# Optimization experiments

Measured on AMD Instinct MI355X. Metric: run time of the kernel, lower is better.

Reference implementation:

```python
import jax, jax.numpy as jnp
import numpy as np

SIZE = 128
WIN = SIZE // 4   # sliding-window size == region size (32)
HALF = WIN // 2   # 16


def _conv(x, w, pad, groups=1):
    return jax.lax.conv_general_dilated(x, w, (1, 1), [(pad, pad), (pad, pad)],
        dimension_numbers=('NCHW', 'OIHW', 'NCHW'), feature_group_count=groups)


def _resize(x, h, w):
    # F.interpolate(..., mode='bilinear', align_corners=False)
    return jax.image.resize(x, (x.shape[0], x.shape[1], h, w), 'bilinear', antialias=False)


def _gauss_kernels():
    ax = np.linspace(-2.0, 2.0, 5)
    xx, yy = np.meshgrid(ax, ax)
    g = np.exp(-(xx ** 2 + yy ** 2) / 2.0) / (2.0 * np.pi)  # sigma = 1
    gx = (-xx * g).astype(np.float32)
    gy = (-yy * g).astype(np.float32)
    return (jnp.asarray(np.tile(gx[None, None], (3, 3, 1, 1))),
            jnp.asarray(np.tile(gy[None, None], (3, 3, 1, 1))))


def _edge_extract(x):
    Gx, Gy = _gauss_kernels()
    h = _conv(x, Gx, 2)
    v = _conv(x, Gy, 2)
    return jnp.tanh(jnp.sqrt(h * h + v * v + 1e-8))


def _color_moments(x, win=5):
    # F.unfold-based local mean / unbiased var / skewness, via depthwise box sums
    C = x.shape[1]
    n = float(win * win)
    ones = jnp.ones((C, 1, win, win), x.dtype)
    box = lambda z: _conv(z, ones, win // 2, groups=C)
    s1 = box(x); s2 = box(x * x); s3 = box(x * x * x)
    mean = s1 / n
    var = (s2 - n * mean * mean) / (n - 1.0)               # unbiased, matches torch.var
    m3 = (s3 - 3.0 * mean * s2 + 2.0 * n * mean ** 3) / n  # E[(x-m)^3]
    skew = m3 / (jnp.sqrt(jnp.maximum(var, 0.0)) ** 3 + 1e-6)
    return jnp.concatenate([mean, var, skew], 1)


def _locate_region(c):
    # scipy: gradient magnitude < 0.2 -> 4-connected label at argmax -> bbox center
    H, W = c.shape
    flat = jnp.argmax(c)
    xm = (flat // W).astype(jnp.int32)
    ym = (flat % W).astype(jnp.int32)
    gm = jnp.hypot(jnp.gradient(c, axis=0), jnp.gradient(c, axis=1))
    mask = gm < 0.2
    seed = jnp.zeros((H, W), bool).at[xm, ym].set(True) & mask

    def dil(r):
        d = r
        d = d | jnp.pad(r[1:, :], ((0, 1), (0, 0)))
        d = d | jnp.pad(r[:-1, :], ((1, 0), (0, 0)))
        d = d | jnp.pad(r[:, 1:], ((0, 0), (0, 1)))
        d = d | jnp.pad(r[:, :-1], ((0, 0), (1, 0)))
        return d & mask

    def body(s):
        r, _ = s
        nr = dil(r)
        return (nr, jnp.any(nr != r))

    region, _ = jax.lax.while_loop(lambda s: s[1], body, (seed, jnp.any(seed)))
    rows = jnp.any(region, 1); cols = jnp.any(region, 0)
    rs = jnp.argmax(rows); re = H - jnp.argmax(rows[::-1])
    cs = jnp.argmax(cols); ce = W - jnp.argmax(cols[::-1])
    ok = mask[xm, ym]  # label_at_max != 0
    x1 = jnp.where(ok, ((rs + re) // 2).astype(jnp.int32), xm)
    y1 = jnp.where(ok, ((cs + ce) // 2).astype(jnp.int32), ym)
    return x1, y1


def _affine_grid(move, H, W):
    # theta = [[1,0,tx],[0,1,ty]] with (tx,ty)=move, align_corners=False
    bx = (2.0 * jnp.arange(W, dtype=jnp.float32) + 1.0) / W - 1.0
    by = (2.0 * jnp.arange(H, dtype=jnp.float32) + 1.0) / H - 1.0
    gx = bx[None, None, :] + move[:, 0, None, None]
    gy = by[None, :, None] + move[:, 1, None, None]
    return jnp.stack(jnp.broadcast_arrays(gx, gy), -1)  # [B,H,W,2]


def _grid_sample(x, grid):
    # bilinear, zeros padding, align_corners=False (torch defaults)
    B, C, H, W = x.shape
    ix = ((grid[..., 0] + 1.0) * W - 1.0) / 2.0
    iy = ((grid[..., 1] + 1.0) * H - 1.0) / 2.0
    ix0 = jnp.floor(ix).astype(jnp.int32)
    iy0 = jnp.floor(iy).astype(jnp.int32)
    wx1 = ix - ix0; wy1 = iy - iy0
    b = jnp.arange(B)[:, None, None]

    def g(yy, xx):
        valid = ((xx >= 0) & (xx < W) & (yy >= 0) & (yy < H)).astype(x.dtype)
        v = x[b, :, jnp.clip(yy, 0, H - 1), jnp.clip(xx, 0, W - 1)]  # [B,Hg,Wg,C]
        return v * valid[..., None]

    out = (g(iy0, ix0) * ((1 - wy1) * (1 - wx1))[..., None]
         + g(iy0, ix0 + 1) * ((1 - wy1) * wx1)[..., None]
         + g(iy0 + 1, ix0) * (wy1 * (1 - wx1))[..., None]
         + g(iy0 + 1, ix0 + 1) * (wy1 * wx1)[..., None])
    return jnp.transpose(out, (0, 3, 1, 2))


def _bn_relu6(x, w, b):
    # BatchNorm2d in training mode (batch stats, biased var, eps=1e-5) + ReLU6
    m = x.mean((0, 2, 3), keepdims=True)
    v = ((x - m) ** 2).mean((0, 2, 3), keepdims=True)
    y = (x - m) / jnp.sqrt(v + 1e-5) * w[None, :, None, None] + b[None, :, None, None]
    return jnp.clip(y, 0.0, 6.0)


def setup_inputs():
    key = jax.random.key(0)
    ks = jax.random.split(key, 8)
    B, C = 8, 64
    return dict(
        warm_flag=1,
        feat1=jax.random.normal(ks[0], (B, C, SIZE, SIZE), jnp.float32),
        feat2=jax.random.normal(ks[1], (B, C, SIZE, SIZE), jnp.float32),
        cam1=jax.random.uniform(ks[2], (B, 64, 64), jnp.float32),
        cam2=jax.random.uniform(ks[3], (B, 64, 64), jnp.float32),
        f_g=jax.random.uniform(ks[4], (B, 3, 512, 512), jnp.float32),
        f_e=jax.random.uniform(ks[5], (B, 3, 512, 512), jnp.float32),
        conv1_w=jax.random.normal(ks[6], (C, 3, 3, 3), jnp.float32) * 0.1,
        conv1_b=jnp.zeros((C,), jnp.float32),
        conv2_w=jax.random.normal(ks[7], (C, 9, 3, 3), jnp.float32) * 0.1,
        conv2_b=jnp.zeros((C,), jnp.float32),
        bn_w=jnp.ones((C,), jnp.float32),
        bn_b=jnp.zeros((C,), jnp.float32),
    )


def reference(warm_flag, feat1, feat2, cam1, cam2, f_g, f_e,
              conv1_w, conv1_b, conv2_w, conv2_b, bn_w, bn_b):
    B = cam1.shape[0]
    c1 = _resize(cam1[:, None], SIZE, SIZE)
    c2 = _resize(cam2[:, None], SIZE, SIZE)

    if warm_flag == 1:
        # numpy/scipy path in torch is detached from autograd
        c1s = jax.lax.stop_gradient(c1)
        c2s = jax.lax.stop_gradient(c2)
        x1, y1 = jax.vmap(_locate_region)(c1s[:, 0])
        # valid-mode box convolution of cam2 with ones((H//4, W//4)), argmax
        box = jax.lax.conv_general_dilated(c2s, jnp.ones((1, 1, WIN, WIN), c2.dtype), (1, 1),
            'VALID', dimension_numbers=('NCHW', 'OIHW', 'NCHW'))[:, 0]
        Wv = box.shape[-1]
        flat = jnp.argmax(box.reshape(B, -1), -1)
        x2 = (flat // Wv + HALF).astype(jnp.int32)
        y2 = (flat % Wv + HALF).astype(jnp.int32)

        idx = jnp.arange(SIZE)
        def rect(xc, yc):
            r = (idx[None, :] >= jnp.maximum(xc - HALF, 0)[:, None]) & \
                (idx[None, :] < jnp.minimum(xc + HALF, SIZE)[:, None])
            cc = (idx[None, :] >= jnp.maximum(yc - HALF, 0)[:, None]) & \
                 (idx[None, :] < jnp.minimum(yc + HALF, SIZE)[:, None])
            return r[:, None, :, None] & cc[:, None, None, :]
        mask1 = rect(x1, y1).astype(feat1.dtype)
        mask2 = rect(x2, y2).astype(feat2.dtype)
        mi1 = jnp.stack([x1, y1], -1).astype(jnp.float32)
        mi2 = jnp.stack([x2, y2], -1).astype(jnp.float32)
    else:
        mask1 = jnp.zeros_like(feat1)
        mask2 = jnp.zeros_like(feat2)
        mi1 = jnp.zeros((B, 2), jnp.float32)
        mi2 = jnp.zeros((B, 2), jnp.float32)

    cam2_move = (mi2 - mi1) / (SIZE // 2)
    cam1_move = (mi1 - mi2) / (SIZE // 2)
    grid1 = _affine_grid(cam1_move, SIZE, SIZE)
    grid2 = _affine_grid(cam2_move, SIZE, SIZE)

    moments = _resize(_color_moments(f_e), SIZE, SIZE)   # [B,9,128,128]
    edge = _resize(_edge_extract(f_g), SIZE, SIZE)       # [B,3,128,128]
    feat1_edge = jnp.clip(_conv(edge, conv1_w, 1) + conv1_b[None, :, None, None], 0.0, 6.0)
    feat2_color = _conv(moments, conv2_w, 1) + conv2_b[None, :, None, None]

    feat2_move = _grid_sample(feat2_color * mask2, grid2)
    feat1_edge_move = _grid_sample(feat1_edge * mask1, grid1)

    Bc, C, H, W = feat1.shape
    f1 = feat1.reshape(Bc, C, -1)
    f2 = feat2.reshape(Bc, C, -1)
    f2m = feat2_move.reshape(Bc, C, -1)
    f1m = feat1_edge_move.reshape(Bc, C, -1)

    f2_attn = jax.nn.softmax(jnp.einsum('bcn,bdn->bcd', f2m, f1), -1)  # [B,C,C]
    feat1_apply = jnp.einsum('bcd,bdn->bcn', f2_attn, f1).reshape(Bc, C, H, W)
    f1_attn = jax.nn.softmax(jnp.einsum('bcn,bdn->bcd', f1m, f2), -1)
    feat2_apply = jnp.einsum('bcd,bdn->bcn', f1_attn, f2).reshape(Bc, C, H, W)

    feat1_apply = _bn_relu6(feat1_apply, bn_w, bn_b)
    feat2_apply = _bn_relu6(feat2_apply, bn_w, bn_b)

    if warm_flag == 0:
        return (feat1, feat2, grid1, grid2, feat1_edge, feat2_color, f1_attn, f2_attn, feat1, feat2)
    return (feat1_apply, feat2_apply, grid1, grid2, feat1_edge, feat2_color, f1_attn, f2_attn, feat1, feat2)
```

## Files before the change

### kernel.cpp

```cpp
#include <hip/hip_runtime.h>
#include <math.h>

#define SIZE 128
#define WIN 32
#define HALF 16
#define B 8
#define C 64
#define N (SIZE*SIZE)
#define BCN 8388608
#define BV 97

#define O_APPLY1   0
#define O_APPLY2   8388608
#define O_GRID1    16777216
#define O_GRID2    17039360
#define O_EDGEF    17301504
#define O_COLORF   25690112
#define O_ATTN1    34078720
#define O_ATTN2    34111488
#define O_FEAT1    34144256
#define O_FEAT2    42532864

#define WS_C1      0
#define WS_C2      131072
#define WS_COLSUM  262144
#define WS_XY      361472
#define WS_MOM     361600
#define WS_EDGE    1541248
#define WS_LOG1    1672320
#define WS_LOG2    1705088
#define WS_BN      1737856

#define NEGINF (-3.402823466e+38f)

typedef unsigned __int128 u128;

__global__ void k_init(float* __restrict__ p, int n) {
  int i = blockIdx.x * 256 + threadIdx.x;
  if (i < n) p[i] = 0.f;
}

__global__ __launch_bounds__(256) void k_resize_cam(
    const float* __restrict__ cam1, const float* __restrict__ cam2,
    float* __restrict__ c1, float* __restrict__ c2) {
  int idx = blockIdx.x * 256 + threadIdx.x;
  int which = idx >> 17;
  int rem = idx & 131071;
  int b = rem >> 14, i = (rem >> 7) & 127, j = rem & 127;
  const float* s = (which ? cam2 : cam1) + b * 4096;
  float fy = fminf(fmaxf(0.5f * (float)i - 0.25f, 0.f), 63.f);
  float fx = fminf(fmaxf(0.5f * (float)j - 0.25f, 0.f), 63.f);
  int y0 = (int)fy; float ty = fy - (float)y0; int y1i = min(y0 + 1, 63);
  int x0 = (int)fx; float tx = fx - (float)x0; int x1i = min(x0 + 1, 63);
  float v00 = s[y0 * 64 + x0],  v01 = s[y0 * 64 + x1i];
  float v10 = s[y1i * 64 + x0], v11 = s[y1i * 64 + x1i];
  float v = (1.f - ty) * ((1.f - tx) * v00 + tx * v01)
          + ty * ((1.f - tx) * v10 + tx * v11);
  (which ? c2 : c1)[rem] = v;
}

__device__ __forceinline__ u128 hfill(u128 g, u128 m) {
  u128 p = m;
  g |= p & (g << 1);  p &= p << 1;
  g |= p & (g << 2);  p &= p << 2;
  g |= p & (g << 4);  p &= p << 4;
  g |= p & (g << 8);  p &= p << 8;
  g |= p & (g << 16); p &= p << 16;
  g |= p & (g << 32); p &= p << 32;
  g |= p & (g << 64);
  p = m;
  g |= p & (g >> 1);  p &= p >> 1;
  g |= p & (g >> 2);  p &= p >> 2;
  g |= p & (g >> 4);  p &= p >> 4;
  g |= p & (g >> 8);  p &= p >> 8;
  g |= p & (g >> 16); p &= p >> 16;
  g |= p & (g >> 32); p &= p >> 32;
  g |= p & (g >> 64);
  return g;
}

__global__ __launch_bounds__(256) void k_locate(const float* __restrict__ c1,
                                                int* __restrict__ xy) {
  int b = blockIdx.x;
  const float* c = c1 + b * N;
  int tid = threadIdx.x;
  __shared__ float sc[N];
  __shared__ float sv[256]; __shared__ int si[256];
  __shared__ unsigned int maskw[512];
  __shared__ unsigned long long glo[128], ghi[128];
  __shared__ unsigned long long rowany[2];
  __shared__ int s_changed, s_xm, s_ym, s_ok;

  float bv = NEGINF; int bi = 0;
  const float4* c4 = (const float4*)c;
  float4* sc4 = (float4*)sc;
  #pragma unroll
  for (int k = 0; k < 16; ++k) {
    int i4 = k * 256 + tid;
    float4 v = c4[i4];
    sc4[i4] = v;
    int base = i4 * 4;
    if (v.x > bv) { bv = v.x; bi = base; }
    if (v.y > bv) { bv = v.y; bi = base + 1; }
    if (v.z > bv) { bv = v.z; bi = base + 2; }
    if (v.w > bv) { bv = v.w; bi = base + 3; }
  }
  sv[tid] = bv; si[tid] = bi;
  __syncthreads();
  for (int s = 128; s; s >>= 1) {
    if (tid < s) {
      float ov = sv[tid + s]; int oi = si[tid + s];
      if (ov > sv[tid] || (ov == sv[tid] && oi < si[tid])) { sv[tid] = ov; si[tid] = oi; }
    }
    __syncthreads();
  }
  if (tid == 0) { s_xm = si[0] >> 7; s_ym = si[0] & 127; }

  #pragma unroll
  for (int q = 0; q < 2; ++q) {
    int w = tid + q * 256;
    int row = w >> 2, cb = (w & 3) * 32;
    unsigned int m = 0;
    for (int bit = 0; bit < 32; ++bit) {
      int i = row, j = cb + bit;
      float gx_, gy_;
      if (i == 0)        gx_ = sc[128 + j] - sc[j];
      else if (i == 127) gx_ = sc[127 * 128 + j] - sc[126 * 128 + j];
      else               gx_ = 0.5f * (sc[(i + 1) * 128 + j] - sc[(i - 1) * 128 + j]);
      if (j == 0)        gy_ = sc[i * 128 + 1] - sc[i * 128];
      else if (j == 127) gy_ = sc[i * 128 + 127] - sc[i * 128 + 126];
      else               gy_ = 0.5f * (sc[i * 128 + j + 1] - sc[i * 128 + j - 1]);
      if (hypotf(gx_, gy_) < 0.2f) m |= (1u << bit);
    }
    maskw[w] = m;
  }
  __syncthreads();
  if (tid == 0) {
    int w = (s_xm << 2) + (s_ym >> 5), bit = s_ym & 31;
    s_ok = (maskw[w] >> bit) & 1;
  }
  __syncthreads();

  int r = tid;
  u128 m = 0, g = 0;
  if (tid < 128) {
    m = ((u128)maskw[r * 4])
      | ((u128)maskw[r * 4 + 1] << 32)
      | ((u128)maskw[r * 4 + 2] << 64)
      | ((u128)maskw[r * 4 + 3] << 96);
    if (s_ok && r == s_xm) g = ((u128)1) << s_ym;
    g = hfill(g, m);
  }
  for (;;) {
    if (tid == 0) s_changed = 0;
    if (tid < 128) { glo[r] = (unsigned long long)g; ghi[r] = (unsigned long long)(g >> 64); }
    __syncthreads();
    if (tid < 128) {
      u128 gn = g;
      if (r > 0)   gn |= ((u128)glo[r - 1]) | ((u128)ghi[r - 1] << 64);
      if (r < 127) gn |= ((u128)glo[r + 1]) | ((u128)ghi[r + 1] << 64);
      gn &= m;
      gn = hfill(gn, m);
      if (gn != g) { g = gn; s_changed = 1; }
    }
    __syncthreads();
    if (!s_changed) break;
  }

  if (tid < 128) {
    unsigned long long ba = __ballot(g != 0);
    if ((tid & 63) == 0) rowany[tid >> 6] = ba;
    glo[r] = (unsigned long long)g; ghi[r] = (unsigned long long)(g >> 64);
  }
  __syncthreads();
  if (tid == 0) {
    unsigned long long r0 = rowany[0], r1 = rowany[1];
    unsigned long long cl = 0, ch = 0;
    for (int i = 0; i < 128; ++i) { cl |= glo[i]; ch |= ghi[i]; }
    int rs = 0, re = 0, cs = 0, ce = 0;
    if (r0 | r1) {
      rs = r0 ? (__ffsll(r0) - 1) : 64 + (__ffsll(r1) - 1);
      re = r1 ? 128 - __clzll(r1) : 64 - __clzll(r0);
      cs = cl ? (__ffsll(cl) - 1) : 64 + (__ffsll(ch) - 1);
      ce = ch ? 128 - __clzll(ch) : 64 - __clzll(cl);
    }
    int x1, y1;
    if (s_ok) { x1 = (rs + re) >> 1; y1 = (cs + ce) >> 1; }
    else      { x1 = s_xm;           y1 = s_ym; }
    xy[b] = x1; xy[8 + b] = y1;
  }
}

__global__ __launch_bounds__(256) void k_colsum(const float* __restrict__ c2,
                                                float* __restrict__ cs) {
  int idx = blockIdx.x * 256 + threadIdx.x;
  if (idx >= B * BV * 128) return;
  int cc = idx & 127, r = (idx >> 7) % BV, b = idx / (BV * 128);
  const float* s = c2 + b * N + cc;
  float acc = 0.f;
  #pragma unroll
  for (int dy = 0; dy < WIN; ++dy) acc += s[(r + dy) * 128];
  cs[idx] = acc;
}

__global__ __launch_bounds__(256) void k_boxargmax(const float* __restrict__ colsum,
                                                   int* __restrict__ xy) {
  int b = blockIdx.x, tid = threadIdx.x;
  const float* cs = colsum + b * BV * 128;
  float bv = NEGINF; int bi = 0;
  for (int p = tid; p < BV * BV; p += 256) {
    int r = p / BV, cc = p % BV;
    const float* row = cs + r * 128 + cc;
    float s = 0.f;
    #pragma unroll
    for (int dx = 0; dx < WIN; ++dx) s += row[dx];
    if (s > bv) { bv = s; bi = p; }
  }
  __shared__ float sv[256]; __shared__ int si[256];
  sv[tid] = bv; si[tid] = bi;
  __syncthreads();
  for (int s = 128; s; s >>= 1) {
    if (tid < s) {
      float ov = sv[tid + s]; int oi = si[tid + s];
      if (ov > sv[tid] || (ov == sv[tid] && oi < si[tid])) { sv[tid] = ov; si[tid] = oi; }
    }
    __syncthreads();
  }
  if (tid == 0) { xy[16 + b] = si[0] / BV + HALF; xy[24 + b] = si[0] % BV + HALF; }
}

__global__ __launch_bounds__(256) void k_grids(const int* __restrict__ xy,
                                               float* __restrict__ g1, float* __restrict__ g2) {
  int idx = blockIdx.x * 256 + threadIdx.x;
  int b = idx >> 14, h = (idx >> 7) & 127, w = idx & 127;
  float x1 = (float)xy[b], y1 = (float)xy[8 + b];
  float x2 = (float)xy[16 + b], y2 = (float)xy[24 + b];
  float bx = (2.f * (float)w + 1.f) / 128.f - 1.f;
  float by = (2.f * (float)h + 1.f) / 128.f - 1.f;
  float m1x = (x1 - x2) / 64.f, m1y = (y1 - y2) / 64.f;
  g1[idx * 2]     = bx + m1x; g1[idx * 2 + 1] = by + m1y;
  g2[idx * 2]     = bx - m1x; g2[idx * 2 + 1] = by - m1y;
}

__global__ __launch_bounds__(256) void k_moments(const float* __restrict__ fe,
                                                 float* __restrict__ mom) {
  int blk = blockIdx.x;
  int tile = blk & 63, ch = (blk >> 6) % 3, b = blk / 192;
  int ti0 = (tile >> 3) * 16, tj0 = (tile & 7) * 16;
  const float* src = fe + (size_t)(b * 3 + ch) * 262144;
  __shared__ float sx[66 * 66];
  int oy0 = 4 * ti0 - 1, ox0 = 4 * tj0 - 1;
  int tid = threadIdx.x;
  for (int l = tid; l < 66 * 66; l += 256) {
    int r = l / 66, cc = l % 66;
    int gy = oy0 + r, gx = ox0 + cc;
    sx[l] = (gy >= 0 && gy < 512 && gx >= 0 && gx < 512) ? src[gy * 512 + gx] : 0.f;
  }
  __syncthreads();
  int ii = tid >> 4, jj = tid & 15;
  int i = ti0 + ii, j = tj0 + jj;
  float s1a[6], s2a[6], s3a[6], s1b[6], s2b[6], s3b[6];
  #pragma unroll
  for (int t = 0; t < 6; ++t) {
    float a1 = 0, a2 = 0, a3 = 0, b1 = 0, b2 = 0, b3 = 0;
    int lx = 4 * jj + t;
    #pragma unroll
    for (int r = 0; r < 6; ++r) {
      float v = sx[(4 * ii + r) * 66 + lx];
      float v2 = v * v, v3 = v2 * v;
      if (r < 5) { a1 += v; a2 += v2; a3 += v3; }
      if (r > 0) { b1 += v; b2 += v2; b3 += v3; }
    }
    s1a[t] = a1; s2a[t] = a2; s3a[t] = a3;
    s1b[t] = b1; s2b[t] = b2; s3b[t] = b3;
  }
  float am = 0, av = 0, as = 0;
  #pragma unroll
  for (int py = 0; py < 2; ++py) {
    #pragma unroll
    for (int px = 0; px < 2; ++px) {
      float s1 = 0, s2 = 0, s3 = 0;
      #pragma unroll
      for (int t = 0; t < 5; ++t) {
        s1 += py ? s1b[px + t] : s1a[px + t];
        s2 += py ? s2b[px + t] : s2a[px + t];
        s3 += py ? s3b[px + t] : s3a[px + t];
      }
      float mean = s1 / 25.f;
      float var  = (s2 - 25.f * mean * mean) / 24.f;
      float m3   = (s3 - 3.f * mean * s2 + 50.f * mean * mean * mean) / 25.f;
      float sq   = sqrtf(fmaxf(var, 0.f));
      float skew = m3 / (sq * sq * sq + 1e-6f);
      am += mean; av += var; as += skew;
    }
  }
  int base = (b * 9 + ch) * N + i * 128 + j;
  mom[base]         = 0.25f * am;
  mom[base + 3 * N] = 0.25f * av;
  mom[base + 6 * N] = 0.25f * as;
}

__global__ __launch_bounds__(256) void k_edge(const float* __restrict__ fg,
                                              float* __restrict__ edge) {
  int blk = blockIdx.x;
  int tile = blk & 63, b = blk >> 6;
  int ti0 = (tile >> 3) * 16, tj0 = (tile & 7) * 16;
  const float* s0 = fg + (size_t)b * 3 * 262144;
  __shared__ float sx[66 * 66];
  int oy0 = 4 * ti0 - 1, ox0 = 4 * tj0 - 1;
  int tid = threadIdx.x;
  for (int l = tid; l < 66 * 66; l += 256) {
    int r = l / 66, cc = l % 66;
    int gy = oy0 + r, gx = ox0 + cc;
    float v = 0.f;
    if (gy >= 0 && gy < 512 && gx >= 0 && gx < 512) {
      int o = gy * 512 + gx;
      v = s0[o] + s0[262144 + o] + s0[524288 + o];
    }
    sx[l] = v;
  }
  __syncthreads();
  int ii = tid >> 4, jj = tid & 15;
  int i = ti0 + ii, j = tj0 + jj;
  const float INV2PI = 0.15915494309189535f;
  float wg[5], ug[5];
  #pragma unroll
  for (int t = 0; t < 5; ++t) {
    float a = (float)t - 2.f;
    float e = expf(-0.5f * a * a);
    wg[t] = e; ug[t] = -a * e;
  }
  float rAa[6], rAb[6], rBa[6], rBb[6];
  #pragma unroll
  for (int t = 0; t < 6; ++t) {
    float aa = 0, ab = 0, ba = 0, bb = 0;
    int lx = 4 * jj + t;
    #pragma unroll
    for (int r = 0; r < 6; ++r) {
      float v = sx[(4 * ii + r) * 66 + lx];
      if (r < 5) { aa += v * wg[r]; ba += v * ug[r]; }
      if (r > 0) { ab += v * wg[r - 1]; bb += v * ug[r - 1]; }
    }
    rAa[t] = aa; rAb[t] = ab; rBa[t] = ba; rBb[t] = bb;
  }
  float acc = 0.f;
  #pragma unroll
  for (int py = 0; py < 2; ++py) {
    #pragma unroll
    for (int px = 0; px < 2; ++px) {
      float h = 0, v = 0;
      #pragma unroll
      for (int t = 0; t < 5; ++t) {
        float A  = py ? rAb[px + t] : rAa[px + t];
        float Bw = py ? rBb[px + t] : rBa[px + t];
        h += A * ug[t];
        v += Bw * wg[t];
      }
      h *= INV2PI; v *= INV2PI;
      acc += tanhf(sqrtf(h * h + v * v + 1e-8f));
    }
  }
  edge[b * N + i * 128 + j] = 0.25f * acc;
}

__global__ __launch_bounds__(256) void k_conv1(const float* __restrict__ edge,
                                               const float* __restrict__ w,
                                               const float* __restrict__ bias,
                                               float* __restrict__ out) {
  int b = blockIdx.x >> 6, tile = blockIdx.x & 63;
  int ti0 = (tile >> 3) * 16, tj0 = (tile & 7) * 16;
  __shared__ float et[18 * 18];
  __shared__ float ws1[64 * 12];
  int tid = threadIdx.x;
  for (int l = tid; l < 324; l += 256) {
    int r = l / 18, cc = l % 18;
    int gi = ti0 + r - 1, gj = tj0 + cc - 1;
    et[l] = (gi >= 0 && gi < 128 && gj >= 0 && gj < 128) ? edge[b * N + gi * 128 + gj] : 0.f;
  }
  for (int l = tid; l < 64 * 12; l += 256) {
    int o = l / 12, t = l % 12;
    ws1[l] = (t < 9) ? (w[o * 27 + t] + w[o * 27 + 9 + t] + w[o * 27 + 18 + t]) : 0.f;
  }
  __syncthreads();
  int i = tid >> 4, j = tid & 15;
  float win[12];
  #pragma unroll
  for (int dy = 0; dy < 3; ++dy)
    #pragma unroll
    for (int dx = 0; dx < 3; ++dx)
      win[dy * 3 + dx] = et[(i + dy) * 18 + (j + dx)];
  win[9] = 0.f; win[10] = 0.f; win[11] = 0.f;
  float* o = out + (size_t)b * C * N + (ti0 + i) * 128 + tj0 + j;
  for (int oc = 0; oc < C; ++oc) {
    const float4* wr = (const float4*)(ws1 + oc * 12);
    float acc = bias[oc];
    #pragma unroll
    for (int q = 0; q < 3; ++q) {
      float4 w4 = wr[q];
      acc += w4.x * win[4 * q] + w4.y * win[4 * q + 1]
           + w4.z * win[4 * q + 2] + w4.w * win[4 * q + 3];
    }
    o[oc * N] = fminf(fmaxf(acc, 0.f), 6.f);
  }
}

__global__ __launch_bounds__(256) void k_conv2(const float* __restrict__ mom,
                                               const float* __restrict__ w,
                                               const float* __restrict__ bias,
                                               float* __restrict__ out) {
  int b = blockIdx.x >> 6, tile = blockIdx.x & 63;
  int ti0 = (tile >> 3) * 16, tj0 = (tile & 7) * 16;
  __shared__ float mt[9 * 324];
  __shared__ float w2s[64 * 84];
  int tid = threadIdx.x;
  for (int l = tid; l < 9 * 324; l += 256) {
    int ic = l / 324, rem = l % 324, r = rem / 18, cc = rem % 18;
    int gi = ti0 + r - 1, gj = tj0 + cc - 1;
    mt[l] = (gi >= 0 && gi < 128 && gj >= 0 && gj < 128) ? mom[(b * 9 + ic) * N + gi * 128 + gj] : 0.f;
  }
  for (int l = tid; l < 64 * 84; l += 256) {
    int o = l / 84, t = l % 84;
    w2s[l] = (t < 81) ? w[o * 81 + t] : 0.f;
  }
  __syncthreads();
  int i = tid >> 4, j = tid & 15;
  float win[84];
  #pragma unroll
  for (int ic = 0; ic < 9; ++ic)
    #pragma unroll
    for (int dy = 0; dy < 3; ++dy)
      #pragma unroll
      for (int dx = 0; dx < 3; ++dx)
        win[ic * 9 + dy * 3 + dx] = mt[ic * 324 + (i + dy) * 18 + (j + dx)];
  win[81] = 0.f; win[82] = 0.f; win[83] = 0.f;
  float* o = out + (size_t)b * C * N + (ti0 + i) * 128 + tj0 + j;
  for (int oc = 0; oc < C; ++oc) {
    const float4* wr = (const float4*)(w2s + oc * 84);
    float acc = bias[oc];
    #pragma unroll
    for (int q = 0; q < 21; ++q) {
      float4 w4 = wr[q];
      acc += w4.x * win[4 * q] + w4.y * win[4 * q + 1]
           + w4.z * win[4 * q + 2] + w4.w * win[4 * q + 3];
    }
    o[oc * N] = acc;
  }
}

__global__ __launch_bounds__(256) void k_logits(const float* __restrict__ aB1,
                                                const float* __restrict__ bB1,
                                                float* __restrict__ out1,
                                                const float* __restrict__ aB2,
                                                const float* __restrict__ bB2,
                                                float* __restrict__ out2,
                                                const int* __restrict__ xy) {
  int mode = blockIdx.y;
  const float* aBase = mode ? aB2 : aB1;
  const float* bBase = mode ? bB2 : bB1;
  float* out = mode ? out2 : out1;
  int b = blockIdx.x >> 4, sl = blockIdx.x & 15;
  int x1 = xy[b], y1 = xy[8 + b], x2 = xy[16 + b], y2 = xy[24 + b];
  int dyh, dxw, rlo, rhi, clo, chi;
  if (mode == 0) {
    dyh = y1 - y2; dxw = x1 - x2;
    rlo = max(x1 - HALF, 0); rhi = min(x1 + HALF, SIZE);
    clo = max(y1 - HALF, 0); chi = min(y1 + HALF, SIZE);
  } else {
    dyh = y2 - y1; dxw = x2 - x1;
    rlo = max(x2 - HALF, 0); rhi = min(x2 + HALF, SIZE);
    clo = max(y2 - HALF, 0); chi = min(y2 + HALF, SIZE);
  }
  int hlo = max(0, rlo - dyh), hhi = min(SIZE, rhi - dyh);
  int wlo = max(0, clo - dxw), whi = min(SIZE, chi - dxw);
  int wn = whi - wlo, hn = hhi - hlo;
  int npos = (wn > 0 && hn > 0) ? wn * hn : 0;
  if (sl * 64 >= npos) return;

  __shared__ float aS[64][65];
  __shared__ float bS[64][65];
  int tid = threadIdx.x;
  const float* aB = aBase + (size_t)b * C * N;
  const float* bB = bBase + (size_t)b * C * N;
  for (int l = tid; l < 4096; l += 256) {
    int ch = l >> 6, k = l & 63;
    int p = sl * 64 + k;
    float av = 0.f, bv = 0.f;
    if (p < npos) {
      int h = hlo + p / wn, w = wlo + p % wn;
      av = aB[ch * N + (h + dyh) * 128 + (w + dxw)];
      bv = bB[ch * N + h * 128 + w];
    }
    aS[ch][k] = av; bS[ch][k] = bv;
  }
  __syncthreads();
  int ci = (tid >> 4) << 2, di = (tid & 15) << 2;
  float acc[4][4] = {};
  #pragma unroll 4
  for (int k = 0; k < 64; ++k) {
    float a0 = aS[ci][k], a1 = aS[ci + 1][k], a2 = aS[ci + 2][k], a3 = aS[ci + 3][k];
    float b0 = bS[di][k], b1 = bS[di + 1][k], b2 = bS[di + 2][k], b3 = bS[di + 3][k];
    acc[0][0] += a0 * b0; acc[0][1] += a0 * b1; acc[0][2] += a0 * b2; acc[0][3] += a0 * b3;
    acc[1][0] += a1 * b0; acc[1][1] += a1 * b1; acc[1][2] += a1 * b2; acc[1][3] += a1 * b3;
    acc[2][0] += a2 * b0; acc[2][1] += a2 * b1; acc[2][2] += a2 * b2; acc[2][3] += a2 * b3;
    acc[3][0] += a3 * b0; acc[3][1] += a3 * b1; acc[3][2] += a3 * b2; acc[3][3] += a3 * b3;
  }
  float* o = out + b * 4096;
  #pragma unroll
  for (int u = 0; u < 4; ++u)
    #pragma unroll
    for (int v = 0; v < 4; ++v)
      atomicAdd(&o[(ci + u) * 64 + (di + v)], acc[u][v]);
}

__global__ void k_softmax(const float* __restrict__ l1, const float* __restrict__ l2,
                          float* __restrict__ o6, float* __restrict__ o7) {
  int row = blockIdx.x;
  const float* src = blockIdx.y ? l2 : l1;
  float* dst = blockIdx.y ? o7 : o6;
  int lane = threadIdx.x;
  float v = src[row * 64 + lane];
  float mx = v;
  for (int off = 32; off; off >>= 1) mx = fmaxf(mx, __shfl_xor(mx, off));
  float e = expf(v - mx);
  float s = e;
  for (int off = 32; off; off >>= 1) s += __shfl_xor(s, off);
  dst[row * 64 + lane] = e / s;
}

__global__ __launch_bounds__(256) void k_apply(const float* __restrict__ a1,
                                               const float* __restrict__ s1_,
                                               float* __restrict__ d1,
                                               const float* __restrict__ a2,
                                               const float* __restrict__ s2_,
                                               float* __restrict__ d2) {
  const float* attn; const float* src; float* dst;
  if (blockIdx.y == 0) { attn = a1; src = s1_; dst = d1; }
  else                 { attn = a2; src = s2_; dst = d2; }
  int b = blockIdx.x >> 6, chunk = blockIdx.x & 63;
  int n0 = chunk * 256 + threadIdx.x;
  const float* s = src + (size_t)b * C * N + n0;
  float v[64];
  #pragma unroll
  for (int d = 0; d < 64; ++d) v[d] = s[d * N];
  const float4* at4 = (const float4*)(attn + b * 4096);
  float* o = dst + (size_t)b * C * N + n0;
  for (int c = 0; c < 64; ++c) {
    float acc = 0.f;
    #pragma unroll
    for (int q = 0; q < 16; ++q) {
      float4 w4 = at4[c * 16 + q];
      acc += w4.x * v[4 * q] + w4.y * v[4 * q + 1] + w4.z * v[4 * q + 2] + w4.w * v[4 * q + 3];
    }
    o[c * N] = acc;
  }
}

__global__ __launch_bounds__(256) void k_bnstats1(const float* __restrict__ t0,
                                                  const float* __restrict__ t1,
                                                  float* __restrict__ part) {
  int c = blockIdx.x, b = blockIdx.y, t = blockIdx.z;
  const float* src = (t ? t1 : t0) + (size_t)(b * C + c) * N;
  const float4* s4 = (const float4*)src;
  float s = 0.f, ss = 0.f;
  #pragma unroll
  for (int k = 0; k < 16; ++k) {
    float4 v = s4[k * 256 + threadIdx.x];
    s  += v.x + v.y + v.z + v.w;
    ss += v.x * v.x + v.y * v.y + v.z * v.z + v.w * v.w;
  }
  for (int off = 32; off; off >>= 1) {
    s  += __shfl_xor(s, off);
    ss += __shfl_xor(ss, off);
  }
  __shared__ float as[4], ass[4];
  int wave = threadIdx.x >> 6;
  if ((threadIdx.x & 63) == 0) { as[wave] = s; ass[wave] = ss; }
  __syncthreads();
  if (threadIdx.x == 0) {
    int idx = (t * C + c) * B + b;
    part[idx]        = as[0] + as[1] + as[2] + as[3];
    part[1024 + idx] = ass[0] + ass[1] + ass[2] + ass[3];
  }
}

__global__ void k_bnstats2(const float* __restrict__ part, float* __restrict__ stats) {
  int i = threadIdx.x;
  int t = i >> 6, c = i & 63;
  float s = 0.f, ss = 0.f;
  #pragma unroll
  for (int b = 0; b < B; ++b) {
    int idx = (t * C + c) * B + b;
    s  += part[idx];
    ss += part[1024 + idx];
  }
  float mean = s / 131072.f;
  float var  = ss / 131072.f - mean * mean;
  stats[t * 128 + c]      = mean;
  stats[t * 128 + 64 + c] = 1.f / sqrtf(var + 1e-5f);
}

__global__ __launch_bounds__(256) void k_bnapply(float* __restrict__ t0, float* __restrict__ t1,
                                                 const float* __restrict__ stats,
                                                 const float* __restrict__ bw,
                                                 const float* __restrict__ bb) {
  int e = blockIdx.x * 256 + threadIdx.x;
  int t = blockIdx.y;
  float* p = t ? t1 : t0;
  int c = (e >> 14) & 63;
  float m = stats[t * 128 + c], r = stats[t * 128 + 64 + c];
  float y = (p[e] - m) * r * bw[c] + bb[c];
  p[e] = fminf(fmaxf(y, 0.f), 6.f);
}

__global__ __launch_bounds__(256) void k_copy2(const float4* __restrict__ s1, float4* __restrict__ d1,
                                               const float4* __restrict__ s2, float4* __restrict__ d2) {
  int i = blockIdx.x * 256 + threadIdx.x;
  d1[i] = s1[i];
  d2[i] = s2[i];
}

extern "C" void kernel_launch(void* const* d_in, const int* in_sizes, int n_in,
                              void* d_out, int out_size, void* d_ws, size_t ws_size,
                              hipStream_t stream) {
  const float* feat1   = (const float*)d_in[1];
  const float* feat2   = (const float*)d_in[2];
  const float* cam1    = (const float*)d_in[3];
  const float* cam2    = (const float*)d_in[4];
  const float* f_g     = (const float*)d_in[5];
  const float* f_e     = (const float*)d_in[6];
  const float* conv1_w = (const float*)d_in[7];
  const float* conv1_b = (const float*)d_in[8];
  const float* conv2_w = (const float*)d_in[9];
  const float* conv2_b = (const float*)d_in[10];
  const float* bn_w    = (const float*)d_in[11];
  const float* bn_b    = (const float*)d_in[12];

  float* out = (float*)d_out;
  float* w = (float*)d_ws;
  int* xy = (int*)(w + WS_XY);

  float* o0 = out + O_APPLY1;
  float* o1 = out + O_APPLY2;
  float* o2 = out + O_GRID1;
  float* o3 = out + O_GRID2;
  float* o4 = out + O_EDGEF;
  float* o5 = out + O_COLORF;
  float* o6 = out + O_ATTN1;
  float* o7 = out + O_ATTN2;
  float* o8 = out + O_FEAT1;
  float* o9 = out + O_FEAT2;

  k_init<<<(65536 + 255) / 256, 256, 0, stream>>>(w + WS_LOG1, 65536);

  k_resize_cam<<<1024, 256, 0, stream>>>(cam1, cam2, w + WS_C1, w + WS_C2);
  k_locate<<<B, 256, 0, stream>>>(w + WS_C1, xy);
  k_colsum<<<(B * BV * 128 + 255) / 256, 256, 0, stream>>>(w + WS_C2, w + WS_COLSUM);
  k_boxargmax<<<B, 256, 0, stream>>>(w + WS_COLSUM, xy);
  k_grids<<<B * N / 256, 256, 0, stream>>>(xy, o2, o3);

  k_moments<<<B * 3 * 64, 256, 0, stream>>>(f_e, w + WS_MOM);
  k_edge<<<B * 64, 256, 0, stream>>>(f_g, w + WS_EDGE);
  k_conv1<<<B * 64, 256, 0, stream>>>(w + WS_EDGE, conv1_w, conv1_b, o4);
  k_conv2<<<B * 64, 256, 0, stream>>>(w + WS_MOM, conv2_w, conv2_b, o5);

  k_copy2<<<BCN / 4 / 256, 256, 0, stream>>>((const float4*)feat1, (float4*)o8,
                                             (const float4*)feat2, (float4*)o9);

  k_logits<<<dim3(B * 16, 2), 256, 0, stream>>>(o4, feat2, w + WS_LOG1,
                                                o5, feat1, w + WS_LOG2, xy);

  k_softmax<<<dim3(B * C, 2), 64, 0, stream>>>(w + WS_LOG1, w + WS_LOG2, o6, o7);

  k_apply<<<dim3(B * 64, 2), 256, 0, stream>>>(o7, feat1, o0, o6, feat2, o1);

  k_bnstats1<<<dim3(C, B, 2), 256, 0, stream>>>(o0, o1, w + WS_LOG1);
  k_bnstats2<<<1, 128, 0, stream>>>(w + WS_LOG1, w + WS_BN);

  k_bnapply<<<dim3(BCN / 256, 2), 256, 0, stream>>>(o0, o1, w + WS_BN, bn_w, bn_b);
}
```

Measured before the change: 640.6 us.

## Fuse front-end, prep, conv, BN-stats and copy kernels into fewer launches

Merges the camera resize, region locate, box-sum argmax and grid generation into one per-batch kernel that keeps everything in shared memory. It also combines the moments and edge kernels, and the two convs, into single launches. BN statistics are now accumulated inside the attention-apply kernel, which removes a full read pass over both outputs. The feature copy is folded into a vectorised BN apply. The front-end now runs on only 8 blocks with large shared memory, which may serialise work that was previously spread across the GPU.

```diff
diff --git a/kernel.cpp b/kernel.cpp
--- a/kernel.cpp
+++ b/kernel.cpp
@@ -21,43 +21,15 @@
 #define O_FEAT1    34144256
 #define O_FEAT2    42532864
 
-#define WS_C1      0
-#define WS_C2      131072
-#define WS_COLSUM  262144
+#define WS_BNP     0
 #define WS_XY      361472
 #define WS_MOM     361600
 #define WS_EDGE    1541248
-#define WS_LOG1    1672320
-#define WS_LOG2    1705088
 #define WS_BN      1737856
 
 #define NEGINF (-3.402823466e+38f)
 
 typedef unsigned __int128 u128;
-
-__global__ void k_init(float* __restrict__ p, int n) {
-  int i = blockIdx.x * 256 + threadIdx.x;
-  if (i < n) p[i] = 0.f;
-}
-
-__global__ __launch_bounds__(256) void k_resize_cam(
-    const float* __restrict__ cam1, const float* __restrict__ cam2,
-    float* __restrict__ c1, float* __restrict__ c2) {
-  int idx = blockIdx.x * 256 + threadIdx.x;
-  int which = idx >> 17;
-  int rem = idx & 131071;
-  int b = rem >> 14, i = (rem >> 7) & 127, j = rem & 127;
-  const float* s = (which ? cam2 : cam1) + b * 4096;
-  float fy = fminf(fmaxf(0.5f * (float)i - 0.25f, 0.f), 63.f);
-  float fx = fminf(fmaxf(0.5f * (float)j - 0.25f, 0.f), 63.f);
-  int y0 = (int)fy; float ty = fy - (float)y0; int y1i = min(y0 + 1, 63);
-  int x0 = (int)fx; float tx = fx - (float)x0; int x1i = min(x0 + 1, 63);
-  float v00 = s[y0 * 64 + x0],  v01 = s[y0 * 64 + x1i];
-  float v10 = s[y1i * 64 + x0], v11 = s[y1i * 64 + x1i];
-  float v = (1.f - ty) * ((1.f - tx) * v00 + tx * v01)
-          + ty * ((1.f - tx) * v10 + tx * v11);
-  (which ? c2 : c1)[rem] = v;
-}
 
 __device__ __forceinline__ u128 hfill(u128 g, u128 m) {
   u128 p = m;
@@ -79,31 +51,40 @@
   return g;
 }
 
-__global__ __launch_bounds__(256) void k_locate(const float* __restrict__ c1,
-                                                int* __restrict__ xy) {
-  int b = blockIdx.x;
-  const float* c = c1 + b * N;
-  int tid = threadIdx.x;
+__global__ __launch_bounds__(256) void k_front(
+    const float* __restrict__ cam1, const float* __restrict__ cam2,
+    int* __restrict__ xy, float* __restrict__ g1, float* __restrict__ g2) {
+  int b = blockIdx.x, tid = threadIdx.x;
   __shared__ float sc[N];
+  __shared__ float sc2[N];
   __shared__ float sv[256]; __shared__ int si[256];
   __shared__ unsigned int maskw[512];
   __shared__ unsigned long long glo[128], ghi[128];
   __shared__ unsigned long long rowany[2];
   __shared__ int s_changed, s_xm, s_ym, s_ok;
+  __shared__ int s_x1, s_y1, s_x2, s_y2;
+
+  const float* src1 = cam1 + b * 4096;
+  const float* src2 = cam2 + b * 4096;
 
   float bv = NEGINF; int bi = 0;
-  const float4* c4 = (const float4*)c;
-  float4* sc4 = (float4*)sc;
-  #pragma unroll
-  for (int k = 0; k < 16; ++k) {
-    int i4 = k * 256 + tid;
-    float4 v = c4[i4];
-    sc4[i4] = v;
-    int base = i4 * 4;
-    if (v.x > bv) { bv = v.x; bi = base; }
-    if (v.y > bv) { bv = v.y; bi = base + 1; }
-    if (v.z > bv) { bv = v.z; bi = base + 2; }
-    if (v.w > bv) { bv = v.w; bi = base + 3; }
+  for (int k = 0; k < 64; ++k) {
+    int pix = k * 256 + tid;
+    int i = pix >> 7, j = pix & 127;
+    float fy = fminf(fmaxf(0.5f * (float)i - 0.25f, 0.f), 63.f);
+    float fx = fminf(fmaxf(0.5f * (float)j - 0.25f, 0.f), 63.f);
+    int y0 = (int)fy; float ty = fy - (float)y0; int y1i = min(y0 + 1, 63);
+    int x0 = (int)fx; float tx = fx - (float)x0; int x1i = min(x0 + 1, 63);
+    float a00 = src1[y0 * 64 + x0],  a01 = src1[y0 * 64 + x1i];
+    float a10 = src1[y1i * 64 + x0], a11 = src1[y1i * 64 + x1i];
+    float v1 = (1.f - ty) * ((1.f - tx) * a00 + tx * a01)
+             + ty * ((1.f - tx) * a10 + tx * a11);
+    float c00 = src2[y0 * 64 + x0],  c01 = src2[y0 * 64 + x1i];
+    float c10 = src2[y1i * 64 + x0], c11 = src2[y1i * 64 + x1i];
+    float v2 = (1.f - ty) * ((1.f - tx) * c00 + tx * c01)
+             + ty * ((1.f - tx) * c10 + tx * c11);
+    sc[pix] = v1; sc2[pix] = v2;
+    if (v1 > bv) { bv = v1; bi = pix; }
   }
   sv[tid] = bv; si[tid] = bi;
   __syncthreads();
@@ -187,36 +168,27 @@
     int x1, y1;
     if (s_ok) { x1 = (rs + re) >> 1; y1 = (cs + ce) >> 1; }
     else      { x1 = s_xm;           y1 = s_ym; }
-    xy[b] = x1; xy[8 + b] = y1;
-  }
-}
-
-__global__ __launch_bounds__(256) void k_colsum(const float* __restrict__ c2,
-                                                float* __restrict__ cs) {
-  int idx = blockIdx.x * 256 + threadIdx.x;
-  if (idx >= B * BV * 128) return;
-  int cc = idx & 127, r = (idx >> 7) % BV, b = idx / (BV * 128);
-  const float* s = c2 + b * N + cc;
-  float acc = 0.f;
-  #pragma unroll
-  for (int dy = 0; dy < WIN; ++dy) acc += s[(r + dy) * 128];
-  cs[idx] = acc;
-}
-
-__global__ __launch_bounds__(256) void k_boxargmax(const float* __restrict__ colsum,
-                                                   int* __restrict__ xy) {
-  int b = blockIdx.x, tid = threadIdx.x;
-  const float* cs = colsum + b * BV * 128;
-  float bv = NEGINF; int bi = 0;
+    xy[b] = x1; xy[8 + b] = y1; s_x1 = x1; s_y1 = y1;
+  }
+  __syncthreads();
+
+  for (int idx = tid; idx < BV * 128; idx += 256) {
+    int rr = idx >> 7, cc = idx & 127;
+    float acc = 0.f;
+    #pragma unroll
+    for (int dy = 0; dy < WIN; ++dy) acc += sc2[(rr + dy) * 128 + cc];
+    sc[idx] = acc;
+  }
+  __syncthreads();
+
+  bv = NEGINF; bi = 0;
   for (int p = tid; p < BV * BV; p += 256) {
-    int r = p / BV, cc = p % BV;
-    const float* row = cs + r * 128 + cc;
+    int rr = p / BV, cc = p % BV;
     float s = 0.f;
     #pragma unroll
-    for (int dx = 0; dx < WIN; ++dx) s += row[dx];
+    for (int dx = 0; dx < WIN; ++dx) s += sc[rr * 128 + cc + dx];
     if (s > bv) { bv = s; bi = p; }
   }
-  __shared__ float sv[256]; __shared__ int si[256];
   sv[tid] = bv; si[tid] = bi;
   __syncthreads();
   for (int s = 128; s; s >>= 1) {
@@ -226,239 +198,237 @@
     }
     __syncthreads();
   }
-  if (tid == 0) { xy[16 + b] = si[0] / BV + HALF; xy[24 + b] = si[0] % BV + HALF; }
-}
-
-__global__ __launch_bounds__(256) void k_grids(const int* __restrict__ xy,
-                                               float* __restrict__ g1, float* __restrict__ g2) {
-  int idx = blockIdx.x * 256 + threadIdx.x;
-  int b = idx >> 14, h = (idx >> 7) & 127, w = idx & 127;
-  float x1 = (float)xy[b], y1 = (float)xy[8 + b];
-  float x2 = (float)xy[16 + b], y2 = (float)xy[24 + b];
-  float bx = (2.f * (float)w + 1.f) / 128.f - 1.f;
-  float by = (2.f * (float)h + 1.f) / 128.f - 1.f;
-  float m1x = (x1 - x2) / 64.f, m1y = (y1 - y2) / 64.f;
-  g1[idx * 2]     = bx + m1x; g1[idx * 2 + 1] = by + m1y;
-  g2[idx * 2]     = bx - m1x; g2[idx * 2 + 1] = by - m1y;
-}
-
-__global__ __launch_bounds__(256) void k_moments(const float* __restrict__ fe,
-                                                 float* __restrict__ mom) {
-  int blk = blockIdx.x;
-  int tile = blk & 63, ch = (blk >> 6) % 3, b = blk / 192;
-  int ti0 = (tile >> 3) * 16, tj0 = (tile & 7) * 16;
-  const float* src = fe + (size_t)(b * 3 + ch) * 262144;
+  if (tid == 0) {
+    int x2 = si[0] / BV + HALF, y2 = si[0] % BV + HALF;
+    xy[16 + b] = x2; xy[24 + b] = y2; s_x2 = x2; s_y2 = y2;
+  }
+  __syncthreads();
+
+  float x1f = (float)s_x1, y1f = (float)s_y1;
+  float x2f = (float)s_x2, y2f = (float)s_y2;
+  float m1x = (x1f - x2f) / 64.f, m1y = (y1f - y2f) / 64.f;
+  float* g1b = g1 + (size_t)b * N * 2;
+  float* g2b = g2 + (size_t)b * N * 2;
+  for (int k = 0; k < 64; ++k) {
+    int pix = k * 256 + tid;
+    int h = pix >> 7, w = pix & 127;
+    float bx = (2.f * (float)w + 1.f) / 128.f - 1.f;
+    float by = (2.f * (float)h + 1.f) / 128.f - 1.f;
+    g1b[pix * 2]     = bx + m1x; g1b[pix * 2 + 1] = by + m1y;
+    g2b[pix * 2]     = bx - m1x; g2b[pix * 2 + 1] = by - m1y;
+  }
+}
+
+__global__ __launch_bounds__(256) void k_prep(const float* __restrict__ fe,
+                                              const float* __restrict__ fg,
+                                              float* __restrict__ mom,
+                                              float* __restrict__ edge) {
   __shared__ float sx[66 * 66];
-  int oy0 = 4 * ti0 - 1, ox0 = 4 * tj0 - 1;
   int tid = threadIdx.x;
-  for (int l = tid; l < 66 * 66; l += 256) {
-    int r = l / 66, cc = l % 66;
-    int gy = oy0 + r, gx = ox0 + cc;
-    sx[l] = (gy >= 0 && gy < 512 && gx >= 0 && gx < 512) ? src[gy * 512 + gx] : 0.f;
-  }
-  __syncthreads();
-  int ii = tid >> 4, jj = tid & 15;
-  int i = ti0 + ii, j = tj0 + jj;
-  float s1a[6], s2a[6], s3a[6], s1b[6], s2b[6], s3b[6];
-  #pragma unroll
-  for (int t = 0; t < 6; ++t) {
-    float a1 = 0, a2 = 0, a3 = 0, b1 = 0, b2 = 0, b3 = 0;
-    int lx = 4 * jj + t;
-    #pragma unroll
-    for (int r = 0; r < 6; ++r) {
-      float v = sx[(4 * ii + r) * 66 + lx];
-      float v2 = v * v, v3 = v2 * v;
-      if (r < 5) { a1 += v; a2 += v2; a3 += v3; }
-      if (r > 0) { b1 += v; b2 += v2; b3 += v3; }
-    }
-    s1a[t] = a1; s2a[t] = a2; s3a[t] = a3;
-    s1b[t] = b1; s2b[t] = b2; s3b[t] = b3;
-  }
-  float am = 0, av = 0, as = 0;
-  #pragma unroll
-  for (int py = 0; py < 2; ++py) {
-    #pragma unroll
-    for (int px = 0; px < 2; ++px) {
-      float s1 = 0, s2 = 0, s3 = 0;
-      #pragma unroll
-      for (int t = 0; t < 5; ++t) {
-        s1 += py ? s1b[px + t] : s1a[px + t];
-        s2 += py ? s2b[px + t] : s2a[px + t];
-        s3 += py ? s3b[px + t] : s3a[px + t];
+  if (blockIdx.x < 1536) {
+    int blk = blockIdx.x;
+    int tile = blk & 63, ch = (blk >> 6) % 3, b = blk / 192;
+    int ti0 = (tile >> 3) * 16, tj0 = (tile & 7) * 16;
+    const float* src = fe + (size_t)(b * 3 + ch) * 262144;
+    int oy0 = 4 * ti0 - 1, ox0 = 4 * tj0 - 1;
+    for (int l = tid; l < 66 * 66; l += 256) {
+      int r = l / 66, cc = l % 66;
+      int gy = oy0 + r, gx = ox0 + cc;
+      sx[l] = (gy >= 0 && gy < 512 && gx >= 0 && gx < 512) ? src[gy * 512 + gx] : 0.f;
+    }
+    __syncthreads();
+    int ii = tid >> 4, jj = tid & 15;
+    int i = ti0 + ii, j = tj0 + jj;
+    float s1a[6], s2a[6], s3a[6], s1b[6], s2b[6], s3b[6];
+    #pragma unroll
+    for (int t = 0; t < 6; ++t) {
+      float a1 = 0, a2 = 0, a3 = 0, b1 = 0, b2 = 0, b3 = 0;
+      int lx = 4 * jj + t;
+      #pragma unroll
+      for (int r = 0; r < 6; ++r) {
+        float v = sx[(4 * ii + r) * 66 + lx];
+        float v2 = v * v, v3 = v2 * v;
+        if (r < 5) { a1 += v; a2 += v2; a3 += v3; }
+        if (r > 0) { b1 += v; b2 += v2; b3 += v3; }
       }
-      float mean = s1 / 25.f;
-      float var  = (s2 - 25.f * mean * mean) / 24.f;
-      float m3   = (s3 - 3.f * mean * s2 + 50.f * mean * mean * mean) / 25.f;
-      float sq   = sqrtf(fmaxf(var, 0.f));
-      float skew = m3 / (sq * sq * sq + 1e-6f);
-      am += mean; av += var; as += skew;
-    }
-  }
-  int base = (b * 9 + ch) * N + i * 128 + j;
-  mom[base]         = 0.25f * am;
-  mom[base + 3 * N] = 0.25f * av;
-  mom[base + 6 * N] = 0.25f * as;
-}
-
-__global__ __launch_bounds__(256) void k_edge(const float* __restrict__ fg,
-                                              float* __restrict__ edge) {
-  int blk = blockIdx.x;
-  int tile = blk & 63, b = blk >> 6;
-  int ti0 = (tile >> 3) * 16, tj0 = (tile & 7) * 16;
-  const float* s0 = fg + (size_t)b * 3 * 262144;
-  __shared__ float sx[66 * 66];
-  int oy0 = 4 * ti0 - 1, ox0 = 4 * tj0 - 1;
-  int tid = threadIdx.x;
-  for (int l = tid; l < 66 * 66; l += 256) {
-    int r = l / 66, cc = l % 66;
-    int gy = oy0 + r, gx = ox0 + cc;
-    float v = 0.f;
-    if (gy >= 0 && gy < 512 && gx >= 0 && gx < 512) {
-      int o = gy * 512 + gx;
-      v = s0[o] + s0[262144 + o] + s0[524288 + o];
-    }
-    sx[l] = v;
-  }
-  __syncthreads();
-  int ii = tid >> 4, jj = tid & 15;
-  int i = ti0 + ii, j = tj0 + jj;
-  const float INV2PI = 0.15915494309189535f;
-  float wg[5], ug[5];
-  #pragma unroll
-  for (int t = 0; t < 5; ++t) {
-    float a = (float)t - 2.f;
-    float e = expf(-0.5f * a * a);
-    wg[t] = e; ug[t] = -a * e;
-  }
-  float rAa[6], rAb[6], rBa[6], rBb[6];
-  #pragma unroll
-  for (int t = 0; t < 6; ++t) {
-    float aa = 0, ab = 0, ba = 0, bb = 0;
-    int lx = 4 * jj + t;
-    #pragma unroll
-    for (int r = 0; r < 6; ++r) {
-      float v = sx[(4 * ii + r) * 66 + lx];
-      if (r < 5) { aa += v * wg[r]; ba += v * ug[r]; }
-      if (r > 0) { ab += v * wg[r - 1]; bb += v * ug[r - 1]; }
-    }
-    rAa[t] = aa; rAb[t] = ab; rBa[t] = ba; rBb[t] = bb;
-  }
-  float acc = 0.f;
-  #pragma unroll
-  for (int py = 0; py < 2; ++py) {
-    #pragma unroll
-    for (int px = 0; px < 2; ++px) {
-      float h = 0, v = 0;
-      #pragma unroll
-      for (int t = 0; t < 5; ++t) {
-        float A  = py ? rAb[px + t] : rAa[px + t];
-        float Bw = py ? rBb[px + t] : rBa[px + t];
-        h += A * ug[t];
-        v += Bw * wg[t];
+      s1a[t] = a1; s2a[t] = a2; s3a[t] = a3;
+      s1b[t] = b1; s2b[t] = b2; s3b[t] = b3;
+    }
+    float am = 0, av = 0, as = 0;
+    #pragma unroll
+    for (int py = 0; py < 2; ++py) {
+      #pragma unroll
+      for (int px = 0; px < 2; ++px) {
+        float s1 = 0, s2 = 0, s3 = 0;
+        #pragma unroll
+        for (int t = 0; t < 5; ++t) {
+          s1 += py ? s1b[px + t] : s1a[px + t];
+          s2 += py ? s2b[px + t] : s2a[px + t];
+          s3 += py ? s3b[px + t] : s3a[px + t];
+        }
+        float mean = s1 / 25.f;
+        float var  = (s2 - 25.f * mean * mean) / 24.f;
+        float m3   = (s3 - 3.f * mean * s2 + 50.f * mean * mean * mean) / 25.f;
+        float sq   = sqrtf(fmaxf(var, 0.f));
+        float skew = m3 / (sq * sq * sq + 1e-6f);
+        am += mean; av += var; as += skew;
       }
-      h *= INV2PI; v *= INV2PI;
-      acc += tanhf(sqrtf(h * h + v * v + 1e-8f));
-    }
-  }
-  edge[b * N + i * 128 + j] = 0.25f * acc;
-}
-
-__global__ __launch_bounds__(256) void k_conv1(const float* __restrict__ edge,
-                                               const float* __restrict__ w,
-                                               const float* __restrict__ bias,
-                                               float* __restrict__ out) {
+    }
+    int base = (b * 9 + ch) * N + i * 128 + j;
+    mom[base]         = 0.25f * am;
+    mom[base + 3 * N] = 0.25f * av;
+    mom[base + 6 * N] = 0.25f * as;
+  } else {
+    int blk = blockIdx.x - 1536;
+    int tile = blk & 63, b = blk >> 6;
+    int ti0 = (tile >> 3) * 16, tj0 = (tile & 7) * 16;
+    const float* s0 = fg + (size_t)b * 3 * 262144;
+    int oy0 = 4 * ti0 - 1, ox0 = 4 * tj0 - 1;
+    for (int l = tid; l < 66 * 66; l += 256) {
+      int r = l / 66, cc = l % 66;
+      int gy = oy0 + r, gx = ox0 + cc;
+      float v = 0.f;
+      if (gy >= 0 && gy < 512 && gx >= 0 && gx < 512) {
+        int o = gy * 512 + gx;
+        v = s0[o] + s0[262144 + o] + s0[524288 + o];
+      }
+      sx[l] = v;
+    }
+    __syncthreads();
+    int ii = tid >> 4, jj = tid & 15;
+    int i = ti0 + ii, j = tj0 + jj;
+    const float INV2PI = 0.15915494309189535f;
+    float wg[5], ug[5];
+    #pragma unroll
+    for (int t = 0; t < 5; ++t) {
+      float a = (float)t - 2.f;
+      float e = expf(-0.5f * a * a);
+      wg[t] = e; ug[t] = -a * e;
+    }
+    float rAa[6], rAb[6], rBa[6], rBb[6];
+    #pragma unroll
+    for (int t = 0; t < 6; ++t) {
+      float aa = 0, ab = 0, ba = 0, bb = 0;
+      int lx = 4 * jj + t;
+      #pragma unroll
+      for (int r = 0; r < 6; ++r) {
+        float v = sx[(4 * ii + r) * 66 + lx];
+        if (r < 5) { aa += v * wg[r]; ba += v * ug[r]; }
+        if (r > 0) { ab += v * wg[r - 1]; bb += v * ug[r - 1]; }
+      }
+      rAa[t] = aa; rAb[t] = ab; rBa[t] = ba; rBb[t] = bb;
+    }
+    float acc = 0.f;
+    #pragma unroll
+    for (int py = 0; py < 2; ++py) {
+      #pragma unroll
+      for (int px = 0; px < 2; ++px) {
+        float h = 0, v = 0;
+        #pragma unroll
+        for (int t = 0; t < 5; ++t) {
+          float A  = py ? rAb[px + t] : rAa[px + t];
+          float Bw = py ? rBb[px + t] : rBa[px + t];
+          h += A * ug[t];
+          v += Bw * wg[t];
+        }
+        h *= INV2PI; v *= INV2PI;
+        acc += tanhf(sqrtf(h * h + v * v + 1e-8f));
+      }
+    }
+    edge[b * N + i * 128 + j] = 0.25f * acc;
+  }
+}
+
+__global__ __launch_bounds__(256) void k_conv12(
+    const float* __restrict__ edge, const float* __restrict__ w1,
+    const float* __restrict__ b1, float* __restrict__ o4,
+    const float* __restrict__ mom, const float* __restrict__ w2,
+    const float* __restrict__ b2, float* __restrict__ o5) {
+  __shared__ float tin[9 * 324];
+  __shared__ float wsm[64 * 84];
   int b = blockIdx.x >> 6, tile = blockIdx.x & 63;
   int ti0 = (tile >> 3) * 16, tj0 = (tile & 7) * 16;
-  __shared__ float et[18 * 18];
-  __shared__ float ws1[64 * 12];
   int tid = threadIdx.x;
-  for (int l = tid; l < 324; l += 256) {
-    int r = l / 18, cc = l % 18;
-    int gi = ti0 + r - 1, gj = tj0 + cc - 1;
-    et[l] = (gi >= 0 && gi < 128 && gj >= 0 && gj < 128) ? edge[b * N + gi * 128 + gj] : 0.f;
-  }
-  for (int l = tid; l < 64 * 12; l += 256) {
-    int o = l / 12, t = l % 12;
-    ws1[l] = (t < 9) ? (w[o * 27 + t] + w[o * 27 + 9 + t] + w[o * 27 + 18 + t]) : 0.f;
-  }
-  __syncthreads();
   int i = tid >> 4, j = tid & 15;
-  float win[12];
-  #pragma unroll
-  for (int dy = 0; dy < 3; ++dy)
-    #pragma unroll
-    for (int dx = 0; dx < 3; ++dx)
-      win[dy * 3 + dx] = et[(i + dy) * 18 + (j + dx)];
-  win[9] = 0.f; win[10] = 0.f; win[11] = 0.f;
-  float* o = out + (size_t)b * C * N + (ti0 + i) * 128 + tj0 + j;
-  for (int oc = 0; oc < C; ++oc) {
-    const float4* wr = (const float4*)(ws1 + oc * 12);
-    float acc = bias[oc];
-    #pragma unroll
-    for (int q = 0; q < 3; ++q) {
-      float4 w4 = wr[q];
-      acc += w4.x * win[4 * q] + w4.y * win[4 * q + 1]
-           + w4.z * win[4 * q + 2] + w4.w * win[4 * q + 3];
-    }
-    o[oc * N] = fminf(fmaxf(acc, 0.f), 6.f);
-  }
-}
-
-__global__ __launch_bounds__(256) void k_conv2(const float* __restrict__ mom,
-                                               const float* __restrict__ w,
-                                               const float* __restrict__ bias,
-                                               float* __restrict__ out) {
-  int b = blockIdx.x >> 6, tile = blockIdx.x & 63;
-  int ti0 = (tile >> 3) * 16, tj0 = (tile & 7) * 16;
-  __shared__ float mt[9 * 324];
-  __shared__ float w2s[64 * 84];
-  int tid = threadIdx.x;
-  for (int l = tid; l < 9 * 324; l += 256) {
-    int ic = l / 324, rem = l % 324, r = rem / 18, cc = rem % 18;
-    int gi = ti0 + r - 1, gj = tj0 + cc - 1;
-    mt[l] = (gi >= 0 && gi < 128 && gj >= 0 && gj < 128) ? mom[(b * 9 + ic) * N + gi * 128 + gj] : 0.f;
-  }
-  for (int l = tid; l < 64 * 84; l += 256) {
-    int o = l / 84, t = l % 84;
-    w2s[l] = (t < 81) ? w[o * 81 + t] : 0.f;
-  }
-  __syncthreads();
-  int i = tid >> 4, j = tid & 15;
-  float win[84];
-  #pragma unroll
-  for (int ic = 0; ic < 9; ++ic)
+  if (blockIdx.y == 0) {
+    for (int l = tid; l < 324; l += 256) {
+      int r = l / 18, cc = l % 18;
+      int gi = ti0 + r - 1, gj = tj0 + cc - 1;
+      tin[l] = (gi >= 0 && gi < 128 && gj >= 0 && gj < 128) ? edge[b * N + gi * 128 + gj] : 0.f;
+    }
+    for (int l = tid; l < 64 * 12; l += 256) {
+      int o = l / 12, t = l % 12;
+      wsm[l] = (t < 9) ? (w1[o * 27 + t] + w1[o * 27 + 9 + t] + w1[o * 27 + 18 + t]) : 0.f;
+    }
+    __syncthreads();
+    float win[12];
     #pragma unroll
     for (int dy = 0; dy < 3; ++dy)
       #pragma unroll
       for (int dx = 0; dx < 3; ++dx)
-        win[ic * 9 + dy * 3 + dx] = mt[ic * 324 + (i + dy) * 18 + (j + dx)];
-  win[81] = 0.f; win[82] = 0.f; win[83] = 0.f;
-  float* o = out + (size_t)b * C * N + (ti0 + i) * 128 + tj0 + j;
-  for (int oc = 0; oc < C; ++oc) {
-    const float4* wr = (const float4*)(w2s + oc * 84);
-    float acc = bias[oc];
-    #pragma unroll
-    for (int q = 0; q < 21; ++q) {
-      float4 w4 = wr[q];
-      acc += w4.x * win[4 * q] + w4.y * win[4 * q + 1]
-           + w4.z * win[4 * q + 2] + w4.w * win[4 * q + 3];
-    }
-    o[oc * N] = acc;
+        win[dy * 3 + dx] = tin[(i + dy) * 18 + (j + dx)];
+    win[9] = 0.f; win[10] = 0.f; win[11] = 0.f;
+    float* o = o4 + (size_t)b * C * N + (ti0 + i) * 128 + tj0 + j;
+    for (int oc = 0; oc < C; ++oc) {
+      const float4* wr = (const float4*)(wsm + oc * 12);
+      float acc = b1[oc];
+      #pragma unroll
+      for (int q = 0; q < 3; ++q) {
+        float4 w4 = wr[q];
+        acc += w4.x * win[4 * q] + w4.y * win[4 * q + 1]
+             + w4.z * win[4 * q + 2] + w4.w * win[4 * q + 3];
+      }
+      o[oc * N] = fminf(fmaxf(acc, 0.f), 6.f);
+    }
+  } else {
+    for (int l = tid; l < 9 * 324; l += 256) {
+      int ic = l / 324, rem = l % 324, r = rem / 18, cc = rem % 18;
+      int gi = ti0 + r - 1, gj = tj0 + cc - 1;
+      tin[l] = (gi >= 0 && gi < 128 && gj >= 0 && gj < 128) ? mom[(b * 9 + ic) * N + gi * 128 + gj] : 0.f;
+    }
+    for (int l = tid; l < 64 * 84; l += 256) {
+      int o = l / 84, t = l % 84;
+      wsm[l] = (t < 81) ? w2[o * 81 + t] : 0.f;
+    }
+    __syncthreads();
+    float win[84];
+    #pragma unroll
+    for (int ic = 0; ic < 9; ++ic)
+      #pragma unroll
+      for (int dy = 0; dy < 3; ++dy)
+        #pragma unroll
+        for (int dx = 0; dx < 3; ++dx)
+          win[ic * 9 + dy * 3 + dx] = tin[ic * 324 + (i + dy) * 18 + (j + dx)];
+    win[81] = 0.f; win[82] = 0.f; win[83] = 0.f;
+    float* o = o5 + (size_t)b * C * N + (ti0 + i) * 128 + tj0 + j;
+    for (int oc = 0; oc < C; ++oc) {
+      const float4* wr = (const float4*)(wsm + oc * 84);
+      float acc = b2[oc];
+      #pragma unroll
+      for (int q = 0; q < 21; ++q) {
+        float4 w4 = wr[q];
+        acc += w4.x * win[4 * q] + w4.y * win[4 * q + 1]
+             + w4.z * win[4 * q + 2] + w4.w * win[4 * q + 3];
+      }
+      o[oc * N] = acc;
+    }
   }
 }
 
 __global__ __launch_bounds__(256) void k_logits(const float* __restrict__ aB1,
                                                 const float* __restrict__ bB1,
-                                                float* __restrict__ out1,
                                                 const float* __restrict__ aB2,
                                                 const float* __restrict__ bB2,
-                                                float* __restrict__ out2,
+                                                float* __restrict__ lg,
                                                 const int* __restrict__ xy) {
   int mode = blockIdx.y;
   const float* aBase = mode ? aB2 : aB1;
   const float* bBase = mode ? bB2 : bB1;
-  float* out = mode ? out2 : out1;
   int b = blockIdx.x >> 4, sl = blockIdx.x & 15;
+  int tid = threadIdx.x;
+  int ci = (tid >> 4) << 2, di = (tid & 15) << 2;
+  float* o = lg + (size_t)(((mode * 8 + b) * 16 + sl)) * 4096;
+
   int x1 = xy[b], y1 = xy[8 + b], x2 = xy[16 + b], y2 = xy[24 + b];
   int dyh, dxw, rlo, rhi, clo, chi;
   if (mode == 0) {
@@ -474,11 +444,17 @@
   int wlo = max(0, clo - dxw), whi = min(SIZE, chi - dxw);
   int wn = whi - wlo, hn = hhi - hlo;
   int npos = (wn > 0 && hn > 0) ? wn * hn : 0;
-  if (sl * 64 >= npos) return;
+  if (sl * 64 >= npos) {
+    #pragma unroll
+    for (int u = 0; u < 4; ++u)
+      #pragma unroll
+      for (int v = 0; v < 4; ++v)
+        o[(ci + u) * 64 + (di + v)] = 0.f;
+    return;
+  }
 
   __shared__ float aS[64][65];
   __shared__ float bS[64][65];
-  int tid = threadIdx.x;
   const float* aB = aBase + (size_t)b * C * N;
   const float* bB = bBase + (size_t)b * C * N;
   for (int l = tid; l < 4096; l += 256) {
@@ -493,32 +469,34 @@
     aS[ch][k] = av; bS[ch][k] = bv;
   }
   __syncthreads();
-  int ci = (tid >> 4) << 2, di = (tid & 15) << 2;
   float acc[4][4] = {};
   #pragma unroll 4
   for (int k = 0; k < 64; ++k) {
     float a0 = aS[ci][k], a1 = aS[ci + 1][k], a2 = aS[ci + 2][k], a3 = aS[ci + 3][k];
-    float b0 = bS[di][k], b1 = bS[di + 1][k], b2 = bS[di + 2][k], b3 = bS[di + 3][k];
-    acc[0][0] += a0 * b0; acc[0][1] += a0 * b1; acc[0][2] += a0 * b2; acc[0][3] += a0 * b3;
-    acc[1][0] += a1 * b0; acc[1][1] += a1 * b1; acc[1][2] += a1 * b2; acc[1][3] += a1 * b3;
-    acc[2][0] += a2 * b0; acc[2][1] += a2 * b1; acc[2][2] += a2 * b2; acc[2][3] += a2 * b3;
-    acc[3][0] += a3 * b0; acc[3][1] += a3 * b1; acc[3][2] += a3 * b2; acc[3][3] += a3 * b3;
-  }
-  float* o = out + b * 4096;
+    float b0 = bS[di][k], b1v = bS[di + 1][k], b2v = bS[di + 2][k], b3 = bS[di + 3][k];
+    acc[0][0] += a0 * b0; acc[0][1] += a0 * b1v; acc[0][2] += a0 * b2v; acc[0][3] += a0 * b3;
+    acc[1][0] += a1 * b0; acc[1][1] += a1 * b1v; acc[1][2] += a1 * b2v; acc[1][3] += a1 * b3;
+    acc[2][0] += a2 * b0; acc[2][1] += a2 * b1v; acc[2][2] += a2 * b2v; acc[2][3] += a2 * b3;
+    acc[3][0] += a3 * b0; acc[3][1] += a3 * b1v; acc[3][2] += a3 * b2v; acc[3][3] += a3 * b3;
+  }
   #pragma unroll
   for (int u = 0; u < 4; ++u)
     #pragma unroll
     for (int v = 0; v < 4; ++v)
-      atomicAdd(&o[(ci + u) * 64 + (di + v)], acc[u][v]);
-}
-
-__global__ void k_softmax(const float* __restrict__ l1, const float* __restrict__ l2,
+      o[(ci + u) * 64 + (di + v)] = acc[u][v];
+}
+
+__global__ void k_softmax(const float* __restrict__ lg,
                           float* __restrict__ o6, float* __restrict__ o7) {
   int row = blockIdx.x;
-  const float* src = blockIdx.y ? l2 : l1;
-  float* dst = blockIdx.y ? o7 : o6;
+  int mode = blockIdx.y;
+  float* dst = mode ? o7 : o6;
+  int b = row >> 6, c = row & 63;
   int lane = threadIdx.x;
-  float v = src[row * 64 + lane];
+  const float* base = lg + (size_t)((mode * 8 + b) * 16) * 4096 + c * 64 + lane;
+  float v = 0.f;
+  #pragma unroll
+  for (int sl = 0; sl < 16; ++sl) v += base[sl * 4096];
   float mx = v;
   for (int off = 32; off; off >>= 1) mx = fmaxf(mx, __shfl_xor(mx, off));
   float e = expf(v - mx);
@@ -527,15 +505,17 @@
   dst[row * 64 + lane] = e / s;
 }
 
-__global__ __launch_bounds__(256) void k_apply(const float* __restrict__ a1,
-                                               const float* __restrict__ s1_,
-                                               float* __restrict__ d1,
-                                               const float* __restrict__ a2,
-                                               const float* __restrict__ s2_,
-                                               float* __restrict__ d2) {
+__global__ __launch_bounds__(256) void k_applyst(const float* __restrict__ a1,
+                                                 const float* __restrict__ s1_,
+                                                 float* __restrict__ d1,
+                                                 const float* __restrict__ a2,
+                                                 const float* __restrict__ s2_,
+                                                 float* __restrict__ d2,
+                                                 float* __restrict__ bnp) {
   const float* attn; const float* src; float* dst;
-  if (blockIdx.y == 0) { attn = a1; src = s1_; dst = d1; }
-  else                 { attn = a2; src = s2_; dst = d2; }
+  int t = blockIdx.y;
+  if (t == 0) { attn = a1; src = s1_; dst = d1; }
+  else        { attn = a2; src = s2_; dst = d2; }
   int b = blockIdx.x >> 6, chunk = blockIdx.x & 63;
   int n0 = chunk * 256 + threadIdx.x;
   const float* s = src + (size_t)b * C * N + n0;
@@ -544,6 +524,8 @@
   for (int d = 0; d < 64; ++d) v[d] = s[d * N];
   const float4* at4 = (const float4*)(attn + b * 4096);
   float* o = dst + (size_t)b * C * N + n0;
+  __shared__ float red[64][4], red2[64][4];
+  int lane = threadIdx.x & 63, wave = threadIdx.x >> 6;
   for (int c = 0; c < 64; ++c) {
     float acc = 0.f;
     #pragma unroll
@@ -552,71 +534,66 @@
       acc += w4.x * v[4 * q] + w4.y * v[4 * q + 1] + w4.z * v[4 * q + 2] + w4.w * v[4 * q + 3];
     }
     o[c * N] = acc;
-  }
-}
-
-__global__ __launch_bounds__(256) void k_bnstats1(const float* __restrict__ t0,
-                                                  const float* __restrict__ t1,
-                                                  float* __restrict__ part) {
-  int c = blockIdx.x, b = blockIdx.y, t = blockIdx.z;
-  const float* src = (t ? t1 : t0) + (size_t)(b * C + c) * N;
-  const float4* s4 = (const float4*)src;
+    float sr = acc, ssr = acc * acc;
+    for (int off = 32; off; off >>= 1) {
+      sr  += __shfl_xor(sr, off);
+      ssr += __shfl_xor(ssr, off);
+    }
+    if (lane == 0) { red[c][wave] = sr; red2[c][wave] = ssr; }
+  }
+  __syncthreads();
+  if (threadIdx.x < 64) {
+    int c = threadIdx.x;
+    float sr  = red[c][0] + red[c][1] + red[c][2] + red[c][3];
+    float ssr = red2[c][0] + red2[c][1] + red2[c][2] + red2[c][3];
+    int idx = (t * 64 + c) * 512 + blockIdx.x;
+    bnp[idx]         = sr;
+    bnp[65536 + idx] = ssr;
+  }
+}
+
+__global__ void k_bnstats2(const float* __restrict__ bnp, float* __restrict__ stats) {
+  __shared__ float sr[128][4], ssr[128][4];
+  int tid = threadIdx.x;
+  int combo = tid >> 2, q = tid & 3;
   float s = 0.f, ss = 0.f;
-  #pragma unroll
-  for (int k = 0; k < 16; ++k) {
-    float4 v = s4[k * 256 + threadIdx.x];
-    s  += v.x + v.y + v.z + v.w;
-    ss += v.x * v.x + v.y * v.y + v.z * v.z + v.w * v.w;
-  }
-  for (int off = 32; off; off >>= 1) {
-    s  += __shfl_xor(s, off);
-    ss += __shfl_xor(ss, off);
-  }
-  __shared__ float as[4], ass[4];
-  int wave = threadIdx.x >> 6;
-  if ((threadIdx.x & 63) == 0) { as[wave] = s; ass[wave] = ss; }
-  __syncthreads();
-  if (threadIdx.x == 0) {
-    int idx = (t * C + c) * B + b;
-    part[idx]        = as[0] + as[1] + as[2] + as[3];
-    part[1024 + idx] = ass[0] + ass[1] + ass[2] + ass[3];
-  }
-}
-
-__global__ void k_bnstats2(const float* __restrict__ part, float* __restrict__ stats) {
-  int i = threadIdx.x;
-  int t = i >> 6, c = i & 63;
-  float s = 0.f, ss = 0.f;
-  #pragma unroll
-  for (int b = 0; b < B; ++b) {
-    int idx = (t * C + c) * B + b;
-    s  += part[idx];
-    ss += part[1024 + idx];
-  }
-  float mean = s / 131072.f;
-  float var  = ss / 131072.f - mean * mean;
-  stats[t * 128 + c]      = mean;
-  stats[t * 128 + 64 + c] = 1.f / sqrtf(var + 1e-5f);
-}
-
-__global__ __launch_bounds__(256) void k_bnapply(float* __restrict__ t0, float* __restrict__ t1,
-                                                 const float* __restrict__ stats,
-                                                 const float* __restrict__ bw,
-                                                 const float* __restrict__ bb) {
-  int e = blockIdx.x * 256 + threadIdx.x;
+  for (int k = 0; k < 128; ++k) {
+    int idx = combo * 512 + q * 128 + k;
+    s  += bnp[idx];
+    ss += bnp[65536 + idx];
+  }
+  sr[combo][q] = s; ssr[combo][q] = ss;
+  __syncthreads();
+  if (q == 0) {
+    float S  = sr[combo][0] + sr[combo][1] + sr[combo][2] + sr[combo][3];
+    float SS = ssr[combo][0] + ssr[combo][1] + ssr[combo][2] + ssr[combo][3];
+    int t = combo >> 6, c = combo & 63;
+    float mean = S / 131072.f;
+    float var  = SS / 131072.f - mean * mean;
+    stats[t * 128 + c]      = mean;
+    stats[t * 128 + 64 + c] = 1.f / sqrtf(var + 1e-5f);
+  }
+}
+
+__global__ __launch_bounds__(256) void k_final(
+    const float4* __restrict__ f1, float4* __restrict__ o8,
+    const float4* __restrict__ f2, float4* __restrict__ o9,
+    float4* __restrict__ o0, float4* __restrict__ o1,
+    const float* __restrict__ stats,
+    const float* __restrict__ bw, const float* __restrict__ bb) {
+  int i = blockIdx.x * 256 + threadIdx.x;
   int t = blockIdx.y;
-  float* p = t ? t1 : t0;
-  int c = (e >> 14) & 63;
+  if (t == 0) o8[i] = f1[i]; else o9[i] = f2[i];
+  float4* p = t ? o1 : o0;
+  int c = (i >> 12) & 63;
   float m = stats[t * 128 + c], r = stats[t * 128 + 64 + c];
-  float y = (p[e] - m) * r * bw[c] + bb[c];
-  p[e] = fminf(fmaxf(y, 0.f), 6.f);
-}
-
-__global__ __launch_bounds__(256) void k_copy2(const float4* __restrict__ s1, float4* __restrict__ d1,
-                                               const float4* __restrict__ s2, float4* __restrict__ d2) {
-  int i = blockIdx.x * 256 + threadIdx.x;
-  d1[i] = s1[i];
-  d2[i] = s2[i];
+  float w_ = bw[c], b_ = bb[c];
+  float4 v = p[i];
+  v.x = fminf(fmaxf((v.x - m) * r * w_ + b_, 0.f), 6.f);
+  v.y = fminf(fmaxf((v.y - m) * r * w_ + b_, 0.f), 6.f);
+  v.z = fminf(fmaxf((v.z - m) * r * w_ + b_, 0.f), 6.f);
+  v.w = fminf(fmaxf((v.w - m) * r * w_ + b_, 0.f), 6.f);
+  p[i] = v;
 }
 
 extern "C" void kernel_launch(void* const* d_in, const int* in_sizes, int n_in,
@@ -650,31 +627,24 @@
   float* o8 = out + O_FEAT1;
   float* o9 = out + O_FEAT2;
 
-  k_init<<<(65536 + 255) / 256, 256, 0, stream>>>(w + WS_LOG1, 65536);
-
-  k_resize_cam<<<1024, 256, 0, stream>>>(cam1, cam2, w + WS_C1, w + WS_C2);
-  k_locate<<<B, 256, 0, stream>>>(w + WS_C1, xy);
-  k_colsum<<<(B * BV * 128 + 255) / 256, 256, 0, stream>>>(w + WS_C2, w + WS_COLSUM);
-  k_boxargmax<<<B, 256, 0, stream>>>(w + WS_COLSUM, xy);
-  k_grids<<<B * N / 256, 256, 0, stream>>>(xy, o2, o3);
-
-  k_moments<<<B * 3 * 64, 256, 0, stream>>>(f_e, w + WS_MOM);
-  k_edge<<<B * 64, 256, 0, stream>>>(f_g, w + WS_EDGE);
-  k_conv1<<<B * 64, 256, 0, stream>>>(w + WS_EDGE, conv1_w, conv1_b, o4);
-  k_conv2<<<B * 64, 256, 0, stream>>>(w + WS_MOM, conv2_w, conv2_b, o5);
-
-  k_copy2<<<BCN / 4 / 256, 256, 0, stream>>>((const float4*)feat1, (float4*)o8,
-                                             (const float4*)feat2, (float4*)o9);
-
-  k_logits<<<dim3(B * 16, 2), 256, 0, stream>>>(o4, feat2, w + WS_LOG1,
-                                                o5, feat1, w + WS_LOG2, xy);
-
-  k_softmax<<<dim3(B * C, 2), 64, 0, stream>>>(w + WS_LOG1, w + WS_LOG2, o6, o7);
-
-  k_apply<<<dim3(B * 64, 2), 256, 0, stream>>>(o7, feat1, o0, o6, feat2, o1);
-
-  k_bnstats1<<<dim3(C, B, 2), 256, 0, stream>>>(o0, o1, w + WS_LOG1);
-  k_bnstats2<<<1, 128, 0, stream>>>(w + WS_LOG1, w + WS_BN);
-
-  k_bnapply<<<dim3(BCN / 256, 2), 256, 0, stream>>>(o0, o1, w + WS_BN, bn_w, bn_b);
-}
+  k_front<<<B, 256, 0, stream>>>(cam1, cam2, xy, o2, o3);
+
+  k_prep<<<2048, 256, 0, stream>>>(f_e, f_g, w + WS_MOM, w + WS_EDGE);
+
+  k_conv12<<<dim3(B * 64, 2), 256, 0, stream>>>(w + WS_EDGE, conv1_w, conv1_b, o4,
+                                                w + WS_MOM, conv2_w, conv2_b, o5);
+
+  k_logits<<<dim3(B * 16, 2), 256, 0, stream>>>(o4, feat2, o5, feat1,
+                                                w + WS_MOM, xy);
+
+  k_softmax<<<dim3(B * C, 2), 64, 0, stream>>>(w + WS_MOM, o6, o7);
+
+  k_applyst<<<dim3(B * 64, 2), 256, 0, stream>>>(o7, feat1, o0, o6, feat2, o1,
+                                                 w + WS_BNP);
+
+  k_bnstats2<<<1, 512, 0, stream>>>(w + WS_BNP, w + WS_BN);
+
+  k_final<<<dim3(BCN / 4 / 256, 2), 256, 0, stream>>>(
+      (const float4*)feat1, (float4*)o8, (const float4*)feat2, (float4*)o9,
+      (float4*)o0, (float4*)o1, w + WS_BN, bn_w, bn_b);
+}
```

Result: no change. 635.6 us (-0.8%).
